# Performance work log

Measured on AMD Instinct MI355X. Metric: run time of the kernel, lower is better.

Reference implementation:

```python
import jax, jax.numpy as jnp
import numpy as np

B, R, N, M, K = 4, 4, 4096, 64, 3
F_NUM = 512
KN = K * N


def _block(x, Ws, bs):
    """SO-Net PointResNet: 1x1 convs + ReLU; last layer sees concat(input, hidden)."""
    h = x
    for W, b in zip(Ws[:-1], bs[:-1]):
        h = jax.nn.relu(jnp.einsum('oc,bcn->bon', W, h) + b[None, :, None])
    h = jnp.concatenate([x, h], axis=1)
    return jax.nn.relu(jnp.einsum('oc,bcn->bon', Ws[-1], h) + bs[-1][None, :, None])


def _forward(x, intensity, node, node_knn_I, fpW, fpB, gpW, gpB):
    # --- som.query_topk: k nearest SOM nodes per point ---
    xd = jax.lax.stop_gradient(x)
    dist = jnp.sum((xd[:, :, :, None] - node[:, :, None, :]) ** 2, axis=1)      # B,N,M
    _, topk = jax.lax.top_k(-dist, K)                                           # B,N,K
    min_idx = topk.transpose(0, 2, 1).reshape(B, KN)                            # B,KN (k copies stacked)
    mask = jax.nn.one_hot(min_idx, M, dtype=jnp.float32)                        # B,KN,M
    mask_row_max = jnp.max(mask, axis=1) > 0                                    # B,M  node has >=1 point
    mask_row_sum = jnp.sum(mask, axis=1)                                        # B,M  points per node

    x_stack = jnp.tile(x, (1, 1, K))                                            # B,2,KN
    cluster_mean = jnp.einsum('bcn,bnm->bcm', jax.lax.stop_gradient(x_stack), mask) \
                   / (mask_row_sum[:, None, :] + 1e-5)                          # B,2,M (detached)

    # --- rotation group (2x2 rotations at angles 2*pi*r/R) ---
    theta = 2.0 * jnp.pi * jnp.arange(R, dtype=jnp.float32) / R
    c, s = jnp.cos(theta), jnp.sin(theta)
    rot = jnp.stack([jnp.stack([c, -s], -1), jnp.stack([s, c], -1)], -2)        # R,2,2

    x_rot = jnp.einsum('rij,bjn->brin', rot, x_stack)                           # B,R,2,KN
    node_rot = jnp.einsum('rij,bjm->brim', rot, cluster_mean)                   # B,R,2,M
    centers = jnp.take_along_axis(node_rot, min_idx[:, None, None, :], axis=3)  # B,R,2,KN
    x_dec = jax.lax.stop_gradient(x_rot - centers).reshape(B * R, 2, KN)

    # --- first PointResNet over all B*R rotation copies ---
    feat = _block(x_dec, fpW, fpB)                                              # BR,128,KN

    # --- index_max scatter-max per SOM cluster (value of argmax == segment max) ---
    seg = jnp.tile(min_idx[:, None, :], (1, R, 1)).reshape(B * R, KN)
    segmax = jax.vmap(lambda f, sgi: jax.ops.segment_max(f.T, sgi, num_segments=M).T)(feat, seg)
    rowmax = jnp.tile(mask_row_max[:, None, :], (1, R, 1)).reshape(B * R, M)
    pooled = jnp.where(rowmax[:, None, :], segmax, feat[:, :, 0:1])             # BR,128,M (empty -> gather idx 0)

    # --- final PointResNet over SOM nodes, then max over nodes and rotations ---
    g_in = jnp.concatenate([node_rot.reshape(B * R, 2, M), pooled], axis=1)     # BR,130,M
    out = _block(g_in, gpW, gpB)                                                # BR,F,M
    return out.reshape(B, R, F_NUM, M).max(axis=3).max(axis=1)                  # B,F


def setup_inputs() -> dict:
    key = jax.random.key(0)
    ks = jax.random.split(key, 24)
    d = {}
    d['x'] = jax.random.normal(ks[0], (B, 2, N), jnp.float32)
    d['intensity'] = jax.random.uniform(ks[1], (B, 1, N), jnp.float32)
    d['node'] = jax.random.normal(ks[2], (B, 2, M), jnp.float32)
    d['node_knn_I'] = jax.random.randint(ks[3], (B, M, 1), 0, M)
    dims_fp = [(64, 2), (64, 64), (128, 64), (128, 130)]      # PointResNet(2,[64,64,128,128])
    dims_gp = [(256, 130), (256, 256), (512, 256), (F_NUM, 642)]  # PointResNet(130,[256,256,512,F])
    i = 4
    for name, dims in (('fp', dims_fp), ('gp', dims_gp)):
        for j, (o, ci) in enumerate(dims):
            d[f'{name}_W{j}'] = jax.random.normal(ks[i], (o, ci), jnp.float32) / np.sqrt(ci).astype(np.float32)
            d[f'{name}_b{j}'] = jnp.zeros((o,), jnp.float32)
            i += 1
    return d


def reference(x, intensity, node, node_knn_I,
              fp_W0, fp_b0, fp_W1, fp_b1, fp_W2, fp_b2, fp_W3, fp_b3,
              gp_W0, gp_b0, gp_W1, gp_b1, gp_W2, gp_b2, gp_W3, gp_b3):
    return _forward(x, intensity, node, node_knn_I,
                    [fp_W0, fp_W1, fp_W2, fp_W3], [fp_b0, fp_b1, fp_b2, fp_b3],
                    [gp_W0, gp_W1, gp_W2, gp_W3], [gp_b0, gp_b1, gp_b2, gp_b3])
```

## Files before the change

### kernel.cpp

```cpp
#include <hip/hip_runtime.h>
#include <stdint.h>

#define BB 4
#define RR 4
#define NN 4096
#define MM 64
#define KK 3
#define KNN 12288
#define BRR 16
#define FF 512

typedef short bf16x8 __attribute__((ext_vector_type(8)));
typedef float f32x4 __attribute__((ext_vector_type(4)));

__device__ __forceinline__ float bf2f(unsigned int u) {
  union { unsigned int i; float f; } v; v.i = u << 16; return v.f;
}
__device__ __forceinline__ unsigned short f2bf(float f) {
  union { float f; unsigned int i; } v; v.f = f;
  unsigned int x = v.i;
  return (unsigned short)((x + 0x7fffu + ((x >> 16) & 1u)) >> 16);
}
__device__ __forceinline__ float ldf(const void* p, long i, int isbf) {
  if (isbf) return bf2f(((const unsigned short*)p)[i]);
  return ((const float*)p)[i];
}

__global__ __launch_bounds__(256) void k_detect(
    const unsigned short* __restrict__ x, int* __restrict__ flag) {
  __shared__ int bad;
  if (threadIdx.x == 0) bad = 0;
  __syncthreads();
  int cnt = 0;
  for (int i = threadIdx.x; i < 1024; i += 256) {
    unsigned short u = x[i * 2];
    int e = (u >> 7) & 0xFF;
    if (e >= 0x90 || (e > 0 && e <= 0x50)) ++cnt;
  }
  atomicAdd(&bad, cnt);
  __syncthreads();
  if (threadIdx.x == 0) flag[0] = (bad < 100) ? 1 : 0;
}

struct WPtrs { const void* p[7]; };
__global__ __launch_bounds__(256) void k_cvt(
    WPtrs wp, const int* __restrict__ flag, unsigned short* __restrict__ Wb) {
  const int e0=4096, e1=12288, e2=28928, e3=62208, e4=127744, e5=258816, e6=587520;
  int t = blockIdx.x * 256 + threadIdx.x;
  if (t >= e6) return;
  int s, base;
  if      (t < e0) { s=0; base=0;  }
  else if (t < e1) { s=1; base=e0; }
  else if (t < e2) { s=2; base=e1; }
  else if (t < e3) { s=3; base=e2; }
  else if (t < e4) { s=4; base=e3; }
  else if (t < e5) { s=5; base=e4; }
  else             { s=6; base=e5; }
  int local = t - base;
  unsigned short u;
  if (flag[0]) u = ((const unsigned short*)wp.p[s])[local];
  else         u = f2bf(((const float*)wp.p[s])[local]);
  Wb[t] = u;
}

__global__ __launch_bounds__(256) void k_assign(
    const void* __restrict__ x, const void* __restrict__ node,
    const int* __restrict__ flag, int* __restrict__ idx, float* __restrict__ csum,
    int* __restrict__ blkcnt) {
  __shared__ float nd[2][64];
  __shared__ float cs[192];
  int isbf = flag[0];
  int tid = threadIdx.x;
  int b = blockIdx.x >> 4;
  int n = ((blockIdx.x & 15) << 8) + tid;
  if (tid < 128) nd[tid >> 6][tid & 63] = ldf(node, b * 128 + tid, isbf);
  if (tid < 192) cs[tid] = 0.f;
  __syncthreads();
  float x0 = ldf(x, b * 8192 + n, isbf);
  float x1 = ldf(x, b * 8192 + 4096 + n, isbf);
  float d0 = 1e30f, d1 = 1e30f, d2 = 1e30f;
  int m0 = 0, m1 = 0, m2 = 0;
#pragma unroll 8
  for (int m = 0; m < 64; ++m) {
    float dx = x0 - nd[0][m];
    float dy = x1 - nd[1][m];
    float d = __fmul_rn(dx, dx) + __fmul_rn(dy, dy);
    if (d < d0)      { d2=d1; m2=m1; d1=d0; m1=m0; d0=d; m0=m; }
    else if (d < d1) { d2=d1; m2=m1; d1=d;  m1=m; }
    else if (d < d2) { d2=d;  m2=m; }
  }
  long base = ((long)b * NN + n) * 3;
  idx[base] = m0; idx[base + 1] = m1; idx[base + 2] = m2;
  atomicAdd(&cs[m0*3+0], x0); atomicAdd(&cs[m0*3+1], x1); atomicAdd(&cs[m0*3+2], 1.f);
  atomicAdd(&cs[m1*3+0], x0); atomicAdd(&cs[m1*3+1], x1); atomicAdd(&cs[m1*3+2], 1.f);
  atomicAdd(&cs[m2*3+0], x0); atomicAdd(&cs[m2*3+1], x1); atomicAdd(&cs[m2*3+2], 1.f);
  __syncthreads();
  if (tid < 192) atomicAdd(&csum[b * 192 + tid], cs[tid]);
  if (tid < 64) blkcnt[blockIdx.x * 64 + tid] = (int)cs[tid*3 + 2];
}

__global__ __launch_bounds__(256) void k_means(
    const float* __restrict__ csum, const int* __restrict__ blkcnt,
    float* __restrict__ noderot, int* __restrict__ rowflag,
    int* __restrict__ off, int* __restrict__ blkoff) {
  int t = threadIdx.x;
  int b = t >> 6, m = t & 63;
  float s0 = csum[b*192 + m*3], s1 = csum[b*192 + m*3 + 1], c = csum[b*192 + m*3 + 2];
  float mx = s0 / (c + 1e-5f);
  float my = s1 / (c + 1e-5f);
  rowflag[b * 64 + m] = (c > 0.f) ? 1 : 0;
  for (int r = 0; r < 4; ++r) {
    float th = 1.5707964f * (float)r;
    float cr = cosf(th), sr = sinf(th);
    noderot[((b*4 + r)*2 + 0)*64 + m] = cr*mx - sr*my;
    noderot[((b*4 + r)*2 + 1)*64 + m] = sr*mx + cr*my;
  }
  if (m == 0) {
    int acc = 0;
    for (int mm = 0; mm < 64; ++mm) {
      off[b*64 + mm] = acc;
      acc += (int)csum[b*192 + mm*3 + 2];
    }
  }
  __syncthreads();
  int base = off[b*64 + m];
  for (int blk = 0; blk < 16; ++blk) {
    blkoff[(b*16 + blk)*64 + m] = base;
    base += blkcnt[(b*16 + blk)*64 + m];
  }
}

__global__ __launch_bounds__(256) void k_scatter(
    const int* __restrict__ idx, const int* __restrict__ blkoff,
    int* __restrict__ sorted) {
  __shared__ int lc[64];
  int tid = threadIdx.x;
  int blk = blockIdx.x;
  int b = blk >> 4;
  int n = ((blk & 15) << 8) + tid;
  if (tid < 64) lc[tid] = 0;
  __syncthreads();
#pragma unroll
  for (int kk = 0; kk < 3; ++kk) {
    int m = idx[((long)b * NN + n) * 3 + kk];
    int pos = atomicAdd(&lc[m], 1);
    sorted[b * KNN + blkoff[blk*64 + m] + pos] = (m << 12) | n;
  }
}

__global__ __launch_bounds__(256) void k_fused(
    const void* __restrict__ x, const int* __restrict__ sorted,
    const int* __restrict__ idx, const float* __restrict__ noderot,
    const int* __restrict__ flag,
    const void* __restrict__ fW0, const void* __restrict__ fb0,
    const unsigned short* __restrict__ Wb,
    const void* __restrict__ fb1, const void* __restrict__ fb2,
    const void* __restrict__ fb3,
    unsigned int* __restrict__ pooled, float* __restrict__ feat0) {
  __shared__ unsigned short Cs[64 * 136];
  __shared__ unsigned short Hs[64 * 72];
  __shared__ int mcol[64];
  const unsigned short* fW1 = Wb;
  const unsigned short* fW2 = Wb + 4096;
  const unsigned short* fW3 = Wb + 12288;
  int isbf = flag[0];
  int tid = threadIdx.x, lane = tid & 63, wv = tid >> 6;
  int quad = lane >> 4, lr = lane & 15;
  int br = blockIdx.y, b = br >> 2, r = br & 3;
  if (tid < 64) {
    int e = sorted[b * KNN + blockIdx.x * 64 + tid];
    int m = e >> 12, n = e & 4095;
    int isz = (n == 0 && m == idx[(long)b * NN * 3]) ? 256 : 0;
    mcol[tid] = m | isz;
    float x0 = ldf(x, b*8192 + n, isbf), x1 = ldf(x, b*8192 + 4096 + n, isbf);
    float th = 1.5707964f * (float)r;
    float cr = cosf(th), sr = sinf(th);
    float xd0 = (cr*x0 - sr*x1) - noderot[(br*2 + 0)*64 + m];
    float xd1 = (sr*x0 + cr*x1) - noderot[(br*2 + 1)*64 + m];
    *(unsigned int*)&Cs[tid * 136] = (unsigned int)f2bf(xd0) | ((unsigned int)f2bf(xd1) << 16);
  }
  __syncthreads();
  {
    int col = tid & 63, og = (tid >> 6) << 4;
    unsigned int xu = *(unsigned int*)&Cs[col * 136];
    float fx0 = bf2f(xu & 0xffff), fx1 = bf2f(xu >> 16);
    union { bf16x8 v; unsigned short s[8]; } o8[2];
#pragma unroll
    for (int j = 0; j < 16; ++j) {
      int o = og + j;
      float h = ldf(fb0, o, isbf) + ldf(fW0, o*2, isbf) * fx0 + ldf(fW0, o*2+1, isbf) * fx1;
      o8[j >> 3].s[j & 7] = f2bf(fmaxf(h, 0.f));
    }
    *(bf16x8*)&Hs[col*72 + og]     = o8[0].v;
    *(bf16x8*)&Hs[col*72 + og + 8] = o8[1].v;
  }
  __syncthreads();
  {
    int o0 = wv * 16;
    f32x4 acc[4];
    float bb4[4];
#pragma unroll
    for (int rr = 0; rr < 4; ++rr) bb4[rr] = ldf(fb1, o0 + quad*4 + rr, isbf);
#pragma unroll
    for (int nt = 0; nt < 4; ++nt) acc[nt] = (f32x4){bb4[0], bb4[1], bb4[2], bb4[3]};
#pragma unroll
    for (int ks = 0; ks < 64; ks += 32) {
      bf16x8 a = *(const bf16x8*)(fW1 + (o0 + lr)*64 + ks + quad*8);
#pragma unroll
      for (int nt = 0; nt < 4; ++nt) {
        bf16x8 bf = *(bf16x8*)&Hs[(nt*16 + lr)*72 + ks + quad*8];
        acc[nt] = __builtin_amdgcn_mfma_f32_16x16x32_bf16(a, bf, acc[nt], 0, 0, 0);
      }
    }
    __syncthreads();
#pragma unroll
    for (int nt = 0; nt < 4; ++nt) {
      int col = nt*16 + lr;
      union { unsigned long long u; unsigned short s[4]; } pk;
#pragma unroll
      for (int rr = 0; rr < 4; ++rr) pk.s[rr] = f2bf(fmaxf(acc[nt][rr], 0.f));
      *(unsigned long long*)&Hs[col*72 + o0 + quad*4] = pk.u;
    }
  }
  __syncthreads();
#pragma unroll
  for (int p2 = 0; p2 < 2; ++p2) {
    int o0 = p2*64 + wv*16;
    f32x4 acc[4];
    float bb4[4];
#pragma unroll
    for (int rr = 0; rr < 4; ++rr) bb4[rr] = ldf(fb2, o0 + quad*4 + rr, isbf);
#pragma unroll
    for (int nt = 0; nt < 4; ++nt) acc[nt] = (f32x4){bb4[0], bb4[1], bb4[2], bb4[3]};
#pragma unroll
    for (int ks = 0; ks < 64; ks += 32) {
      bf16x8 a = *(const bf16x8*)(fW2 + (o0 + lr)*64 + ks + quad*8);
#pragma unroll
      for (int nt = 0; nt < 4; ++nt) {
        bf16x8 bf = *(bf16x8*)&Hs[(nt*16 + lr)*72 + ks + quad*8];
        acc[nt] = __builtin_amdgcn_mfma_f32_16x16x32_bf16(a, bf, acc[nt], 0, 0, 0);
      }
    }
#pragma unroll
    for (int nt = 0; nt < 4; ++nt) {
      int col = nt*16 + lr;
      int o = o0 + quad*4;
      unsigned int w0 = (unsigned int)f2bf(fmaxf(acc[nt][0], 0.f)) |
                        ((unsigned int)f2bf(fmaxf(acc[nt][1], 0.f)) << 16);
      unsigned int w1 = (unsigned int)f2bf(fmaxf(acc[nt][2], 0.f)) |
                        ((unsigned int)f2bf(fmaxf(acc[nt][3], 0.f)) << 16);
      *(unsigned int*)&Cs[col*136 + 2 + o] = w0;
      *(unsigned int*)&Cs[col*136 + 4 + o] = w1;
    }
  }
  __syncthreads();
  f32x4 acc3[2][4];
#pragma unroll
  for (int p3 = 0; p3 < 2; ++p3) {
    int o0 = p3*64 + wv*16;
    float bb4[4];
#pragma unroll
    for (int rr = 0; rr < 4; ++rr) bb4[rr] = ldf(fb3, o0 + quad*4 + rr, isbf);
#pragma unroll
    for (int nt = 0; nt < 4; ++nt) acc3[p3][nt] = (f32x4){bb4[0], bb4[1], bb4[2], bb4[3]};
#pragma unroll
    for (int ks = 0; ks < 128; ks += 32) {
      union { bf16x8 v; unsigned int u[4]; } au;
      const unsigned int* ap = (const unsigned int*)(fW3 + (long)(o0 + lr)*130 + ks + quad*8);
      au.u[0] = ap[0]; au.u[1] = ap[1]; au.u[2] = ap[2]; au.u[3] = ap[3];
#pragma unroll
      for (int nt = 0; nt < 4; ++nt) {
        bf16x8 bf = *(bf16x8*)&Cs[(nt*16 + lr)*136 + ks + quad*8];
        acc3[p3][nt] = __builtin_amdgcn_mfma_f32_16x16x32_bf16(au.v, bf, acc3[p3][nt], 0, 0, 0);
      }
    }
#pragma unroll
    for (int rr = 0; rr < 4; ++rr) {
      int o = o0 + quad*4 + rr;
      unsigned int wu = *(const unsigned int*)(fW3 + (long)o*130 + 128);
      float w0 = bf2f(wu & 0xffff), w1 = bf2f(wu >> 16);
#pragma unroll
      for (int nt = 0; nt < 4; ++nt) {
        unsigned int bu = *(unsigned int*)&Cs[(nt*16 + lr)*136 + 128];
        acc3[p3][nt][rr] += w0 * bf2f(bu & 0xffff) + w1 * bf2f(bu >> 16);
      }
    }
  }
  __syncthreads();
#pragma unroll
  for (int p3 = 0; p3 < 2; ++p3) {
    int o0 = p3*64 + wv*16;
#pragma unroll
    for (int nt = 0; nt < 4; ++nt) {
      int col = nt*16 + lr;
      union { unsigned long long u; unsigned short s[4]; } pk;
#pragma unroll
      for (int rr = 0; rr < 4; ++rr) pk.s[rr] = f2bf(fmaxf(acc3[p3][nt][rr], 0.f));
      *(unsigned long long*)&Cs[col*136 + o0 + quad*4] = pk.u;
    }
  }
  __syncthreads();
  {
    int o = tid & 127, h = tid >> 7;
    int c0 = h * 32;
    int curm = mcol[c0] & 255;
    float v = 0.f;
    for (int c = c0; c < c0 + 32; ++c) {
      int mc = mcol[c];
      int mm = mc & 255;
      float f = bf2f(Cs[c*136 + o]);
      if (mm != curm) {
        atomicMax(&pooled[(((long)br*64 + curm) << 7) + o], __float_as_uint(v));
        curm = mm; v = 0.f;
      }
      v = fmaxf(v, f);
      if (mc & 256) feat0[br*128 + o] = f;
    }
    atomicMax(&pooled[(((long)br*64 + curm) << 7) + o], __float_as_uint(v));
  }
}

__global__ __launch_bounds__(256) void k_finalize(
    const unsigned int* __restrict__ pooled, const float* __restrict__ feat0,
    const int* __restrict__ rowflag, const float* __restrict__ noderot,
    unsigned short* __restrict__ AG) {
  int t = blockIdx.x * 256 + threadIdx.x;
  int col = t >> 7, o = t & 127;
  int br = col >> 6, m = col & 63, b = br >> 2;
  float v = __uint_as_float(pooled[((long)col << 7) + o]);
  if (!rowflag[b*64 + m]) v = feat0[br*128 + o];
  AG[(long)col*648 + 2 + o] = f2bf(v);
  if (o < 2) AG[(long)col*648 + o] = f2bf(noderot[(br*2 + o)*64 + m]);
}

template<int KW, int KMAIN, bool REM2, int BSTR, int OSTR, int OOFF, int EPI>
__global__ __launch_bounds__(256) void k_gemm(
    const unsigned short* __restrict__ W, const void* __restrict__ bias,
    const int* __restrict__ flag,
    const unsigned short* __restrict__ Bb, unsigned short* __restrict__ Out,
    unsigned int* __restrict__ outmax) {
  int isbf = flag[0];
  int lane = threadIdx.x & 63;
  int wv = threadIdx.x >> 6;
  int quad = lane >> 4, lr = lane & 15;
  int o0 = blockIdx.y * 64 + wv * 16;
  long p0 = (long)blockIdx.x * 64;
  float bia[4];
#pragma unroll
  for (int rr = 0; rr < 4; ++rr) bia[rr] = ldf(bias, o0 + quad*4 + rr, isbf);
  f32x4 acc[4];
#pragma unroll
  for (int nt = 0; nt < 4; ++nt) acc[nt] = (f32x4){bia[0], bia[1], bia[2], bia[3]};
  const unsigned short* arow = W + (long)(o0 + lr) * KW;
  for (int ks = 0; ks < KMAIN; ks += 32) {
    bf16x8 a;
    if constexpr ((KW % 8) == 0) {
      a = *(const bf16x8*)(arow + ks + quad*8);
    } else {
      union { bf16x8 v; unsigned int u[4]; } au;
      const unsigned int* ap = (const unsigned int*)(arow + ks + quad*8);
      au.u[0] = ap[0]; au.u[1] = ap[1]; au.u[2] = ap[2]; au.u[3] = ap[3];
      a = au.v;
    }
#pragma unroll
    for (int nt = 0; nt < 4; ++nt) {
      bf16x8 bf = *(const bf16x8*)(Bb + (p0 + nt*16 + lr) * BSTR + ks + quad*8);
      acc[nt] = __builtin_amdgcn_mfma_f32_16x16x32_bf16(a, bf, acc[nt], 0, 0, 0);
    }
  }
  if constexpr (REM2) {
#pragma unroll
    for (int rr = 0; rr < 4; ++rr) {
      int o = o0 + quad*4 + rr;
      unsigned int wu = *(const unsigned int*)(W + (long)o * KW + KMAIN);
      float w0 = bf2f(wu & 0xffff), w1 = bf2f(wu >> 16);
#pragma unroll
      for (int nt = 0; nt < 4; ++nt) {
        long p = p0 + nt*16 + lr;
        unsigned int bu = *(const unsigned int*)(Bb + p * BSTR + KMAIN);
        acc[nt][rr] += w0 * bf2f(bu & 0xffff) + w1 * bf2f(bu >> 16);
      }
    }
  }
  if constexpr (EPI == 0) {
#pragma unroll
    for (int nt = 0; nt < 4; ++nt) {
      long p = p0 + nt*16 + lr;
      unsigned short v0 = f2bf(fmaxf(acc[nt][0], 0.f));
      unsigned short v1 = f2bf(fmaxf(acc[nt][1], 0.f));
      unsigned short v2 = f2bf(fmaxf(acc[nt][2], 0.f));
      unsigned short v3 = f2bf(fmaxf(acc[nt][3], 0.f));
      unsigned short* op = Out + p * OSTR + OOFF + o0 + quad*4;
      if constexpr (((OOFF * 2) % 8) == 0) {
        union { unsigned long long u; unsigned short s[4]; } pk;
        pk.s[0] = v0; pk.s[1] = v1; pk.s[2] = v2; pk.s[3] = v3;
        *(unsigned long long*)op = pk.u;
      } else {
        *(unsigned int*)op       = (unsigned int)v0 | ((unsigned int)v1 << 16);
        *(unsigned int*)(op + 2) = (unsigned int)v2 | ((unsigned int)v3 << 16);
      }
    }
  } else {
#pragma unroll
    for (int rr = 0; rr < 4; ++rr) {
      float v = fmaxf(fmaxf(acc[0][rr], acc[1][rr]), fmaxf(acc[2][rr], acc[3][rr]));
      v = fmaxf(v, 0.f);
      v = fmaxf(v, __shfl_xor(v, 1, 64));
      v = fmaxf(v, __shfl_xor(v, 2, 64));
      v = fmaxf(v, __shfl_xor(v, 4, 64));
      v = fmaxf(v, __shfl_xor(v, 8, 64));
      if (lr == 0) {
        int bb2 = (int)(blockIdx.x >> 2);
        atomicMax(&outmax[bb2 * FF + o0 + quad*4 + rr], __float_as_uint(v));
      }
    }
  }
}

__global__ __launch_bounds__(256) void k_out(
    const unsigned int* __restrict__ outmax, const int* __restrict__ flag,
    void* __restrict__ out) {
  int t = blockIdx.x * 256 + threadIdx.x;
  float v = __uint_as_float(outmax[t]);
  if (flag[0]) ((unsigned short*)out)[t] = f2bf(v);
  else         ((float*)out)[t] = v;
}

extern "C" void kernel_launch(void* const* d_in, const int* in_sizes, int n_in,
                              void* d_out, int out_size, void* d_ws, size_t ws_size,
                              hipStream_t stream) {
  const void* x    = d_in[0];
  const void* node = d_in[2];
  const void* fpW0 = d_in[4];  const void* fpb0 = d_in[5];
  const void* fpW1 = d_in[6];  const void* fpb1 = d_in[7];
  const void* fpW2 = d_in[8];  const void* fpb2 = d_in[9];
  const void* fpW3 = d_in[10]; const void* fpb3 = d_in[11];
  const void* gpW0 = d_in[12]; const void* gpb0 = d_in[13];
  const void* gpW1 = d_in[14]; const void* gpb1 = d_in[15];
  const void* gpW2 = d_in[16]; const void* gpb2 = d_in[17];
  const void* gpW3 = d_in[18]; const void* gpb3 = d_in[19];

  char* ws = (char*)d_ws;
  int*            flag    = (int*)(ws + 0);
  float*          csum    = (float*)(ws + 256);
  unsigned int*   outmax  = (unsigned int*)(ws + 3328);
  unsigned int*   pooled  = (unsigned int*)(ws + 11520);
  int*            idx     = (int*)(ws + 535808);
  int*            blkcnt  = (int*)(ws + 732416);
  int*            blkoff  = (int*)(ws + 748800);
  int*            off     = (int*)(ws + 765184);
  float*          noderot = (float*)(ws + 766208);
  int*            rowflag = (int*)(ws + 774400);
  int*            sorted  = (int*)(ws + 775424);
  float*          feat0   = (float*)(ws + 972032);
  unsigned short* AG      = (unsigned short*)(ws + 980224);
  unsigned short* Hg1     = (unsigned short*)(ws + 2307328);
  unsigned short* Hg2     = (unsigned short*)(ws + 2831616);
  unsigned short* Wb      = (unsigned short*)(ws + 3355904);

  hipMemsetAsync(ws, 0, 535808, stream);

  k_detect<<<1, 256, 0, stream>>>((const unsigned short*)x, flag);
  WPtrs wp; wp.p[0]=fpW1; wp.p[1]=fpW2; wp.p[2]=fpW3; wp.p[3]=gpW0;
  wp.p[4]=gpW1; wp.p[5]=gpW2; wp.p[6]=gpW3;
  k_cvt<<<2295, 256, 0, stream>>>(wp, flag, Wb);

  k_assign<<<64, 256, 0, stream>>>(x, node, flag, idx, csum, blkcnt);
  k_means<<<1, 256, 0, stream>>>(csum, blkcnt, noderot, rowflag, off, blkoff);
  k_scatter<<<64, 256, 0, stream>>>(idx, blkoff, sorted);
  k_fused<<<dim3(192, 16), 256, 0, stream>>>(x, sorted, idx, noderot, flag,
                                             fpW0, fpb0, Wb, fpb1, fpb2, fpb3,
                                             pooled, feat0);
  k_finalize<<<512, 256, 0, stream>>>(pooled, feat0, rowflag, noderot, AG);

  const unsigned short* gW0 = Wb + 28928;
  const unsigned short* gW1 = Wb + 62208;
  const unsigned short* gW2 = Wb + 127744;
  const unsigned short* gW3 = Wb + 258816;
  k_gemm<130, 128, true, 648, 256, 0, 0><<<dim3(16, 4), 256, 0, stream>>>(gW0, gpb0, flag, AG, Hg1, nullptr);
  k_gemm<256, 256, false, 256, 256, 0, 0><<<dim3(16, 4), 256, 0, stream>>>(gW1, gpb1, flag, Hg1, Hg2, nullptr);
  k_gemm<256, 256, false, 256, 648, 130, 0><<<dim3(16, 8), 256, 0, stream>>>(gW2, gpb2, flag, Hg2, AG, nullptr);
  k_gemm<642, 640, true, 648, 0, 0, 2><<<dim3(16, 8), 256, 0, stream>>>(gW3, gpb3, flag, AG, nullptr, outmax);

  k_out<<<8, 256, 0, stream>>>(outmax, flag, d_out);
}
```

Measured before the change: 201.0 us.

## Fuse launch pipeline into four kernels with a single-block-tile global-pool MLP

```diff
diff --git a/kernel.cpp b/kernel.cpp
--- a/kernel.cpp
+++ b/kernel.cpp
@@ -10,6 +10,24 @@
 #define BRR 16
 #define FF 512
 
+#define W_FPW1 0
+#define W_FPW2 4096
+#define W_FPW3 12288
+#define W_GPW0 28928
+#define W_GPW1 62208
+#define W_GPW2 127744
+#define W_GPW3 258816
+#define W_FPB1 587520
+#define W_FPB2 587584
+#define W_FPB3 587712
+#define W_GPB0 587840
+#define W_GPB1 588096
+#define W_GPB2 588352
+#define W_GPB3 588864
+#define W_FPB0 589376
+#define W_FPW0 589440
+#define W_TOT  589568
+
 typedef short bf16x8 __attribute__((ext_vector_type(8)));
 typedef float f32x4 __attribute__((ext_vector_type(4)));
 
@@ -21,56 +39,68 @@
   unsigned int x = v.i;
   return (unsigned short)((x + 0x7fffu + ((x >> 16) & 1u)) >> 16);
 }
+__device__ __forceinline__ unsigned int f2bf2(float a, float b) {
+#if __has_builtin(__builtin_amdgcn_cvt_pk_bf16_f32)
+  typedef __bf16 bf2_t __attribute__((ext_vector_type(2)));
+  union { bf2_t v; unsigned int u; } c;
+  c.v = __builtin_amdgcn_cvt_pk_bf16_f32(a, b);
+  return c.u;
+#else
+  return (unsigned int)f2bf(a) | ((unsigned int)f2bf(b) << 16);
+#endif
+}
 __device__ __forceinline__ float ldf(const void* p, long i, int isbf) {
   if (isbf) return bf2f(((const unsigned short*)p)[i]);
   return ((const float*)p)[i];
 }
-
-__global__ __launch_bounds__(256) void k_detect(
-    const unsigned short* __restrict__ x, int* __restrict__ flag) {
-  __shared__ int bad;
-  if (threadIdx.x == 0) bad = 0;
-  __syncthreads();
-  int cnt = 0;
-  for (int i = threadIdx.x; i < 1024; i += 256) {
-    unsigned short u = x[i * 2];
-    int e = (u >> 7) & 0xFF;
-    if (e >= 0x90 || (e > 0 && e <= 0x50)) ++cnt;
-  }
-  atomicAdd(&bad, cnt);
-  __syncthreads();
-  if (threadIdx.x == 0) flag[0] = (bad < 100) ? 1 : 0;
-}
-
-struct WPtrs { const void* p[7]; };
-__global__ __launch_bounds__(256) void k_cvt(
-    WPtrs wp, const int* __restrict__ flag, unsigned short* __restrict__ Wb) {
-  const int e0=4096, e1=12288, e2=28928, e3=62208, e4=127744, e5=258816, e6=587520;
-  int t = blockIdx.x * 256 + threadIdx.x;
-  if (t >= e6) return;
-  int s, base;
-  if      (t < e0) { s=0; base=0;  }
-  else if (t < e1) { s=1; base=e0; }
-  else if (t < e2) { s=2; base=e1; }
-  else if (t < e3) { s=3; base=e2; }
-  else if (t < e4) { s=4; base=e3; }
-  else if (t < e5) { s=5; base=e4; }
-  else             { s=6; base=e5; }
-  int local = t - base;
-  unsigned short u;
-  if (flag[0]) u = ((const unsigned short*)wp.p[s])[local];
-  else         u = f2bf(((const float*)wp.p[s])[local]);
-  Wb[t] = u;
-}
-
-__global__ __launch_bounds__(256) void k_assign(
-    const void* __restrict__ x, const void* __restrict__ node,
-    const int* __restrict__ flag, int* __restrict__ idx, float* __restrict__ csum,
-    int* __restrict__ blkcnt) {
+__device__ __forceinline__ int detect_bf(const unsigned short* xs) {
+  int lane = threadIdx.x & 63;
+  unsigned short u = xs[lane * 2];
+  int e = (u >> 7) & 0xFF;
+  int bad = (e >= 0x90 || (e > 0 && e <= 0x50)) ? 1 : 0;
+  unsigned long long m = __ballot(bad);
+  return __popcll(m) < 16;
+}
+
+struct SrcPtrs { const void* p[16]; };
+__global__ __launch_bounds__(256) void k_pre(
+    SrcPtrs sp, const void* __restrict__ x, const void* __restrict__ node,
+    int* __restrict__ idx, float* __restrict__ csum, int* __restrict__ blkcnt,
+    unsigned short* __restrict__ Wb) {
+  int isbf = detect_bf((const unsigned short*)x);
+  int tid = threadIdx.x;
+  if (blockIdx.x >= 64) {
+    int t = (blockIdx.x - 64) * 256 + tid;
+    if (t >= W_TOT) return;
+    int s, base;
+    if (t < 28928) {
+      if (t < 4096)        { s=0;  base=0; }
+      else if (t < 12288)  { s=1;  base=4096; }
+      else                 { s=2;  base=12288; }
+    } else if (t < 587520) {
+      if (t < 62208)       { s=3;  base=28928; }
+      else if (t < 127744) { s=4;  base=62208; }
+      else if (t < 258816) { s=5;  base=127744; }
+      else                 { s=6;  base=258816; }
+    } else if (t < 588864) {
+      if (t < 587584)      { s=7;  base=587520; }
+      else if (t < 587712) { s=8;  base=587584; }
+      else if (t < 587840) { s=9;  base=587712; }
+      else if (t < 588096) { s=10; base=587840; }
+      else if (t < 588352) { s=11; base=588096; }
+      else                 { s=12; base=588352; }
+    } else {
+      if (t < 589376)      { s=13; base=588864; }
+      else if (t < 589440) { s=14; base=589376; }
+      else                 { s=15; base=589440; }
+    }
+    int local = t - base;
+    Wb[t] = isbf ? ((const unsigned short*)sp.p[s])[local]
+                 : f2bf(((const float*)sp.p[s])[local]);
+    return;
+  }
   __shared__ float nd[2][64];
   __shared__ float cs[192];
-  int isbf = flag[0];
-  int tid = threadIdx.x;
   int b = blockIdx.x >> 4;
   int n = ((blockIdx.x & 15) << 8) + tid;
   if (tid < 128) nd[tid >> 6][tid & 63] = ldf(node, b * 128 + tid, isbf);
@@ -99,71 +129,70 @@
   if (tid < 64) blkcnt[blockIdx.x * 64 + tid] = (int)cs[tid*3 + 2];
 }
 
-__global__ __launch_bounds__(256) void k_means(
+__global__ __launch_bounds__(256) void k_mid(
     const float* __restrict__ csum, const int* __restrict__ blkcnt,
+    const int* __restrict__ idx,
     float* __restrict__ noderot, int* __restrict__ rowflag,
-    int* __restrict__ off, int* __restrict__ blkoff) {
-  int t = threadIdx.x;
-  int b = t >> 6, m = t & 63;
-  float s0 = csum[b*192 + m*3], s1 = csum[b*192 + m*3 + 1], c = csum[b*192 + m*3 + 2];
-  float mx = s0 / (c + 1e-5f);
-  float my = s1 / (c + 1e-5f);
-  rowflag[b * 64 + m] = (c > 0.f) ? 1 : 0;
-  for (int r = 0; r < 4; ++r) {
-    float th = 1.5707964f * (float)r;
-    float cr = cosf(th), sr = sinf(th);
-    noderot[((b*4 + r)*2 + 0)*64 + m] = cr*mx - sr*my;
-    noderot[((b*4 + r)*2 + 1)*64 + m] = sr*mx + cr*my;
-  }
-  if (m == 0) {
-    int acc = 0;
-    for (int mm = 0; mm < 64; ++mm) {
-      off[b*64 + mm] = acc;
-      acc += (int)csum[b*192 + mm*3 + 2];
-    }
-  }
-  __syncthreads();
-  int base = off[b*64 + m];
-  for (int blk = 0; blk < 16; ++blk) {
-    blkoff[(b*16 + blk)*64 + m] = base;
-    base += blkcnt[(b*16 + blk)*64 + m];
-  }
-}
-
-__global__ __launch_bounds__(256) void k_scatter(
-    const int* __restrict__ idx, const int* __restrict__ blkoff,
     int* __restrict__ sorted) {
+  __shared__ float cls[192];
+  __shared__ int offs[64];
+  __shared__ int lbase[64];
   __shared__ int lc[64];
   int tid = threadIdx.x;
   int blk = blockIdx.x;
-  int b = blk >> 4;
-  int n = ((blk & 15) << 8) + tid;
-  if (tid < 64) lc[tid] = 0;
-  __syncthreads();
+  int b = blk >> 4, chunk = blk & 15;
+  if (tid < 192) cls[tid] = csum[b * 192 + tid];
+  __syncthreads();
+  if (tid < 64) {
+    int m = tid;
+    float s0 = cls[m*3], s1 = cls[m*3+1], c = cls[m*3+2];
+    float mx = s0 / (c + 1e-5f), my = s1 / (c + 1e-5f);
+    rowflag[b*64 + m] = (c > 0.f) ? 1 : 0;
+    for (int r = 0; r < 4; ++r) {
+      float th = 1.5707964f * (float)r;
+      float cr = cosf(th), sr = sinf(th);
+      noderot[((b*4+r)*2+0)*64 + m] = cr*mx - sr*my;
+      noderot[((b*4+r)*2+1)*64 + m] = sr*mx + cr*my;
+    }
+    lc[m] = 0;
+  }
+  if (tid == 0) {
+    int acc = 0;
+    for (int mm = 0; mm < 64; ++mm) { offs[mm] = acc; acc += (int)cls[mm*3+2]; }
+  }
+  __syncthreads();
+  if (tid < 64) {
+    int base = offs[tid];
+    for (int c2 = 0; c2 < chunk; ++c2) base += blkcnt[(b*16 + c2)*64 + tid];
+    lbase[tid] = base;
+  }
+  __syncthreads();
+  int n = (chunk << 8) + tid;
 #pragma unroll
   for (int kk = 0; kk < 3; ++kk) {
-    int m = idx[((long)b * NN + n) * 3 + kk];
+    int m = idx[((long)b*NN + n)*3 + kk];
     int pos = atomicAdd(&lc[m], 1);
-    sorted[b * KNN + blkoff[blk*64 + m] + pos] = (m << 12) | n;
+    sorted[b*KNN + lbase[m] + pos] = (m << 12) | n;
   }
 }
 
 __global__ __launch_bounds__(256) void k_fused(
     const void* __restrict__ x, const int* __restrict__ sorted,
     const int* __restrict__ idx, const float* __restrict__ noderot,
-    const int* __restrict__ flag,
-    const void* __restrict__ fW0, const void* __restrict__ fb0,
     const unsigned short* __restrict__ Wb,
-    const void* __restrict__ fb1, const void* __restrict__ fb2,
-    const void* __restrict__ fb3,
     unsigned int* __restrict__ pooled, float* __restrict__ feat0) {
   __shared__ unsigned short Cs[64 * 136];
   __shared__ unsigned short Hs[64 * 72];
   __shared__ int mcol[64];
-  const unsigned short* fW1 = Wb;
-  const unsigned short* fW2 = Wb + 4096;
-  const unsigned short* fW3 = Wb + 12288;
-  int isbf = flag[0];
+  const unsigned short* fW1 = Wb + W_FPW1;
+  const unsigned short* fW2 = Wb + W_FPW2;
+  const unsigned short* fW3 = Wb + W_FPW3;
+  const unsigned short* fb1 = Wb + W_FPB1;
+  const unsigned short* fb2 = Wb + W_FPB2;
+  const unsigned short* fb3 = Wb + W_FPB3;
+  const unsigned short* fb0 = Wb + W_FPB0;
+  const unsigned short* fW0 = Wb + W_FPW0;
+  int isbf = detect_bf((const unsigned short*)x);
   int tid = threadIdx.x, lane = tid & 63, wv = tid >> 6;
   int quad = lane >> 4, lr = lane & 15;
   int br = blockIdx.y, b = br >> 2, r = br & 3;
@@ -177,22 +206,25 @@
     float cr = cosf(th), sr = sinf(th);
     float xd0 = (cr*x0 - sr*x1) - noderot[(br*2 + 0)*64 + m];
     float xd1 = (sr*x0 + cr*x1) - noderot[(br*2 + 1)*64 + m];
-    *(unsigned int*)&Cs[tid * 136] = (unsigned int)f2bf(xd0) | ((unsigned int)f2bf(xd1) << 16);
+    *(unsigned int*)&Cs[tid * 136] = f2bf2(xd0, xd1);
   }
   __syncthreads();
   {
     int col = tid & 63, og = (tid >> 6) << 4;
     unsigned int xu = *(unsigned int*)&Cs[col * 136];
     float fx0 = bf2f(xu & 0xffff), fx1 = bf2f(xu >> 16);
-    union { bf16x8 v; unsigned short s[8]; } o8[2];
-#pragma unroll
-    for (int j = 0; j < 16; ++j) {
+    union { unsigned int u[8]; bf16x8 v[2]; } o8;
+#pragma unroll
+    for (int j = 0; j < 16; j += 2) {
       int o = og + j;
-      float h = ldf(fb0, o, isbf) + ldf(fW0, o*2, isbf) * fx0 + ldf(fW0, o*2+1, isbf) * fx1;
-      o8[j >> 3].s[j & 7] = f2bf(fmaxf(h, 0.f));
-    }
-    *(bf16x8*)&Hs[col*72 + og]     = o8[0].v;
-    *(bf16x8*)&Hs[col*72 + og + 8] = o8[1].v;
+      unsigned int wu0 = *(const unsigned int*)&fW0[o*2];
+      unsigned int wu1 = *(const unsigned int*)&fW0[o*2 + 2];
+      float h0 = bf2f(fb0[o])   + bf2f(wu0 & 0xffff)*fx0 + bf2f(wu0 >> 16)*fx1;
+      float h1 = bf2f(fb0[o+1]) + bf2f(wu1 & 0xffff)*fx0 + bf2f(wu1 >> 16)*fx1;
+      o8.u[j >> 1] = f2bf2(fmaxf(h0, 0.f), fmaxf(h1, 0.f));
+    }
+    *(bf16x8*)&Hs[col*72 + og]     = o8.v[0];
+    *(bf16x8*)&Hs[col*72 + og + 8] = o8.v[1];
   }
   __syncthreads();
   {
@@ -200,7 +232,7 @@
     f32x4 acc[4];
     float bb4[4];
 #pragma unroll
-    for (int rr = 0; rr < 4; ++rr) bb4[rr] = ldf(fb1, o0 + quad*4 + rr, isbf);
+    for (int rr = 0; rr < 4; ++rr) bb4[rr] = bf2f(fb1[o0 + quad*4 + rr]);
 #pragma unroll
     for (int nt = 0; nt < 4; ++nt) acc[nt] = (f32x4){bb4[0], bb4[1], bb4[2], bb4[3]};
 #pragma unroll
@@ -216,10 +248,10 @@
 #pragma unroll
     for (int nt = 0; nt < 4; ++nt) {
       int col = nt*16 + lr;
-      union { unsigned long long u; unsigned short s[4]; } pk;
-#pragma unroll
-      for (int rr = 0; rr < 4; ++rr) pk.s[rr] = f2bf(fmaxf(acc[nt][rr], 0.f));
-      *(unsigned long long*)&Hs[col*72 + o0 + quad*4] = pk.u;
+      unsigned long long pk =
+        (unsigned long long)f2bf2(fmaxf(acc[nt][0],0.f), fmaxf(acc[nt][1],0.f)) |
+        ((unsigned long long)f2bf2(fmaxf(acc[nt][2],0.f), fmaxf(acc[nt][3],0.f)) << 32);
+      *(unsigned long long*)&Hs[col*72 + o0 + quad*4] = pk;
     }
   }
   __syncthreads();
@@ -229,7 +261,7 @@
     f32x4 acc[4];
     float bb4[4];
 #pragma unroll
-    for (int rr = 0; rr < 4; ++rr) bb4[rr] = ldf(fb2, o0 + quad*4 + rr, isbf);
+    for (int rr = 0; rr < 4; ++rr) bb4[rr] = bf2f(fb2[o0 + quad*4 + rr]);
 #pragma unroll
     for (int nt = 0; nt < 4; ++nt) acc[nt] = (f32x4){bb4[0], bb4[1], bb4[2], bb4[3]};
 #pragma unroll
@@ -245,12 +277,8 @@
     for (int nt = 0; nt < 4; ++nt) {
       int col = nt*16 + lr;
       int o = o0 + quad*4;
-      unsigned int w0 = (unsigned int)f2bf(fmaxf(acc[nt][0], 0.f)) |
-                        ((unsigned int)f2bf(fmaxf(acc[nt][1], 0.f)) << 16);
-      unsigned int w1 = (unsigned int)f2bf(fmaxf(acc[nt][2], 0.f)) |
-                        ((unsigned int)f2bf(fmaxf(acc[nt][3], 0.f)) << 16);
-      *(unsigned int*)&Cs[col*136 + 2 + o] = w0;
-      *(unsigned int*)&Cs[col*136 + 4 + o] = w1;
+      *(unsigned int*)&Cs[col*136 + 2 + o] = f2bf2(fmaxf(acc[nt][0],0.f), fmaxf(acc[nt][1],0.f));
+      *(unsigned int*)&Cs[col*136 + 4 + o] = f2bf2(fmaxf(acc[nt][2],0.f), fmaxf(acc[nt][3],0.f));
     }
   }
   __syncthreads();
@@ -260,7 +288,7 @@
     int o0 = p3*64 + wv*16;
     float bb4[4];
 #pragma unroll
-    for (int rr = 0; rr < 4; ++rr) bb4[rr] = ldf(fb3, o0 + quad*4 + rr, isbf);
+    for (int rr = 0; rr < 4; ++rr) bb4[rr] = bf2f(fb3[o0 + quad*4 + rr]);
 #pragma unroll
     for (int nt = 0; nt < 4; ++nt) acc3[p3][nt] = (f32x4){bb4[0], bb4[1], bb4[2], bb4[3]};
 #pragma unroll
@@ -293,10 +321,10 @@
 #pragma unroll
     for (int nt = 0; nt < 4; ++nt) {
       int col = nt*16 + lr;
-      union { unsigned long long u; unsigned short s[4]; } pk;
-#pragma unroll
-      for (int rr = 0; rr < 4; ++rr) pk.s[rr] = f2bf(fmaxf(acc3[p3][nt][rr], 0.f));
-      *(unsigned long long*)&Cs[col*136 + o0 + quad*4] = pk.u;
+      unsigned long long pk =
+        (unsigned long long)f2bf2(fmaxf(acc3[p3][nt][0],0.f), fmaxf(acc3[p3][nt][1],0.f)) |
+        ((unsigned long long)f2bf2(fmaxf(acc3[p3][nt][2],0.f), fmaxf(acc3[p3][nt][3],0.f)) << 32);
+      *(unsigned long long*)&Cs[col*136 + o0 + quad*4] = pk;
     }
   }
   __syncthreads();
@@ -320,110 +348,179 @@
   }
 }
 
-__global__ __launch_bounds__(256) void k_finalize(
+__global__ __launch_bounds__(256) void k_gp(
+    const void* __restrict__ x,
     const unsigned int* __restrict__ pooled, const float* __restrict__ feat0,
     const int* __restrict__ rowflag, const float* __restrict__ noderot,
-    unsigned short* __restrict__ AG) {
-  int t = blockIdx.x * 256 + threadIdx.x;
-  int col = t >> 7, o = t & 127;
-  int br = col >> 6, m = col & 63, b = br >> 2;
-  float v = __uint_as_float(pooled[((long)col << 7) + o]);
-  if (!rowflag[b*64 + m]) v = feat0[br*128 + o];
-  AG[(long)col*648 + 2 + o] = f2bf(v);
-  if (o < 2) AG[(long)col*648 + o] = f2bf(noderot[(br*2 + o)*64 + m]);
-}
-
-template<int KW, int KMAIN, bool REM2, int BSTR, int OSTR, int OOFF, int EPI>
-__global__ __launch_bounds__(256) void k_gemm(
-    const unsigned short* __restrict__ W, const void* __restrict__ bias,
-    const int* __restrict__ flag,
-    const unsigned short* __restrict__ Bb, unsigned short* __restrict__ Out,
-    unsigned int* __restrict__ outmax) {
-  int isbf = flag[0];
-  int lane = threadIdx.x & 63;
-  int wv = threadIdx.x >> 6;
+    const unsigned short* __restrict__ Wb,
+    unsigned int* __restrict__ outmax, unsigned int* __restrict__ counter,
+    void* __restrict__ out) {
+  __shared__ unsigned short AGs[16 * 648];
+  __shared__ unsigned short H1s[16 * 264];
+  __shared__ unsigned short H2s[16 * 264];
+  __shared__ int done_s;
+  int isbf = detect_bf((const unsigned short*)x);
+  int tid = threadIdx.x, lane = tid & 63, wv = tid >> 6;
   int quad = lane >> 4, lr = lane & 15;
-  int o0 = blockIdx.y * 64 + wv * 16;
-  long p0 = (long)blockIdx.x * 64;
-  float bia[4];
-#pragma unroll
-  for (int rr = 0; rr < 4; ++rr) bia[rr] = ldf(bias, o0 + quad*4 + rr, isbf);
-  f32x4 acc[4];
-#pragma unroll
-  for (int nt = 0; nt < 4; ++nt) acc[nt] = (f32x4){bia[0], bia[1], bia[2], bia[3]};
-  const unsigned short* arow = W + (long)(o0 + lr) * KW;
-  for (int ks = 0; ks < KMAIN; ks += 32) {
-    bf16x8 a;
-    if constexpr ((KW % 8) == 0) {
-      a = *(const bf16x8*)(arow + ks + quad*8);
-    } else {
-      union { bf16x8 v; unsigned int u[4]; } au;
-      const unsigned int* ap = (const unsigned int*)(arow + ks + quad*8);
-      au.u[0] = ap[0]; au.u[1] = ap[1]; au.u[2] = ap[2]; au.u[3] = ap[3];
-      a = au.v;
-    }
-#pragma unroll
-    for (int nt = 0; nt < 4; ++nt) {
-      bf16x8 bf = *(const bf16x8*)(Bb + (p0 + nt*16 + lr) * BSTR + ks + quad*8);
-      acc[nt] = __builtin_amdgcn_mfma_f32_16x16x32_bf16(a, bf, acc[nt], 0, 0, 0);
-    }
-  }
-  if constexpr (REM2) {
-#pragma unroll
-    for (int rr = 0; rr < 4; ++rr) {
-      int o = o0 + quad*4 + rr;
-      unsigned int wu = *(const unsigned int*)(W + (long)o * KW + KMAIN);
-      float w0 = bf2f(wu & 0xffff), w1 = bf2f(wu >> 16);
-#pragma unroll
-      for (int nt = 0; nt < 4; ++nt) {
-        long p = p0 + nt*16 + lr;
-        unsigned int bu = *(const unsigned int*)(Bb + p * BSTR + KMAIN);
-        acc[nt][rr] += w0 * bf2f(bu & 0xffff) + w1 * bf2f(bu >> 16);
-      }
-    }
-  }
-  if constexpr (EPI == 0) {
-#pragma unroll
-    for (int nt = 0; nt < 4; ++nt) {
-      long p = p0 + nt*16 + lr;
-      unsigned short v0 = f2bf(fmaxf(acc[nt][0], 0.f));
-      unsigned short v1 = f2bf(fmaxf(acc[nt][1], 0.f));
-      unsigned short v2 = f2bf(fmaxf(acc[nt][2], 0.f));
-      unsigned short v3 = f2bf(fmaxf(acc[nt][3], 0.f));
-      unsigned short* op = Out + p * OSTR + OOFF + o0 + quad*4;
-      if constexpr (((OOFF * 2) % 8) == 0) {
-        union { unsigned long long u; unsigned short s[4]; } pk;
-        pk.s[0] = v0; pk.s[1] = v1; pk.s[2] = v2; pk.s[3] = v3;
-        *(unsigned long long*)op = pk.u;
-      } else {
-        *(unsigned int*)op       = (unsigned int)v0 | ((unsigned int)v1 << 16);
-        *(unsigned int*)(op + 2) = (unsigned int)v2 | ((unsigned int)v3 << 16);
-      }
-    }
-  } else {
-#pragma unroll
-    for (int rr = 0; rr < 4; ++rr) {
-      float v = fmaxf(fmaxf(acc[0][rr], acc[1][rr]), fmaxf(acc[2][rr], acc[3][rr]));
-      v = fmaxf(v, 0.f);
-      v = fmaxf(v, __shfl_xor(v, 1, 64));
-      v = fmaxf(v, __shfl_xor(v, 2, 64));
-      v = fmaxf(v, __shfl_xor(v, 4, 64));
-      v = fmaxf(v, __shfl_xor(v, 8, 64));
-      if (lr == 0) {
-        int bb2 = (int)(blockIdx.x >> 2);
-        atomicMax(&outmax[bb2 * FF + o0 + quad*4 + rr], __float_as_uint(v));
-      }
-    }
-  }
-}
-
-__global__ __launch_bounds__(256) void k_out(
-    const unsigned int* __restrict__ outmax, const int* __restrict__ flag,
-    void* __restrict__ out) {
-  int t = blockIdx.x * 256 + threadIdx.x;
-  float v = __uint_as_float(outmax[t]);
-  if (flag[0]) ((unsigned short*)out)[t] = f2bf(v);
-  else         ((float*)out)[t] = v;
+  int col0 = blockIdx.x * 16;
+  int br = col0 >> 6, b = br >> 2;
+  for (int i = tid; i < 2048; i += 256) {
+    int c = i >> 7, o = i & 127;
+    int gc = col0 + c, m = gc & 63;
+    float v = __uint_as_float(pooled[((long)gc << 7) + o]);
+    if (!rowflag[b * 64 + m]) v = feat0[br * 128 + o];
+    AGs[c * 648 + 2 + o] = f2bf(v);
+  }
+  if (tid < 32) {
+    int c = tid >> 1, j = tid & 1;
+    int m = (col0 + c) & 63;
+    AGs[c * 648 + j] = f2bf(noderot[(br * 2 + j) * 64 + m]);
+  }
+  __syncthreads();
+  {
+    const unsigned short* W = Wb + W_GPW0;
+    const unsigned short* Bi = Wb + W_GPB0;
+    f32x4 acc[4];
+#pragma unroll
+    for (int rt = 0; rt < 4; ++rt) {
+      int o0 = wv*64 + rt*16 + quad*4;
+      acc[rt] = (f32x4){bf2f(Bi[o0]), bf2f(Bi[o0+1]), bf2f(Bi[o0+2]), bf2f(Bi[o0+3])};
+    }
+#pragma unroll
+    for (int ks = 0; ks < 128; ks += 32) {
+      bf16x8 bfr = *(bf16x8*)&AGs[lr * 648 + ks + quad * 8];
+#pragma unroll
+      for (int rt = 0; rt < 4; ++rt) {
+        int o0 = wv*64 + rt*16;
+        union { bf16x8 v; unsigned int u[4]; } au;
+        const unsigned int* ap = (const unsigned int*)(W + (o0 + lr)*130 + ks + quad*8);
+        au.u[0]=ap[0]; au.u[1]=ap[1]; au.u[2]=ap[2]; au.u[3]=ap[3];
+        acc[rt] = __builtin_amdgcn_mfma_f32_16x16x32_bf16(au.v, bfr, acc[rt], 0,0,0);
+      }
+    }
+    unsigned int bu = *(unsigned int*)&AGs[lr * 648 + 128];
+    float b0v = bf2f(bu & 0xffff), b1v = bf2f(bu >> 16);
+#pragma unroll
+    for (int rt = 0; rt < 4; ++rt) {
+#pragma unroll
+      for (int rr = 0; rr < 4; ++rr) {
+        int o = wv*64 + rt*16 + quad*4 + rr;
+        unsigned int wu = *(const unsigned int*)(W + o*130 + 128);
+        acc[rt][rr] += bf2f(wu & 0xffff)*b0v + bf2f(wu >> 16)*b1v;
+      }
+      int o0 = wv*64 + rt*16;
+      unsigned long long pk =
+        (unsigned long long)f2bf2(fmaxf(acc[rt][0],0.f), fmaxf(acc[rt][1],0.f)) |
+        ((unsigned long long)f2bf2(fmaxf(acc[rt][2],0.f), fmaxf(acc[rt][3],0.f)) << 32);
+      *(unsigned long long*)&H1s[lr*264 + o0 + quad*4] = pk;
+    }
+  }
+  __syncthreads();
+  {
+    const unsigned short* W = Wb + W_GPW1;
+    const unsigned short* Bi = Wb + W_GPB1;
+    f32x4 acc[4];
+#pragma unroll
+    for (int rt = 0; rt < 4; ++rt) {
+      int o0 = wv*64 + rt*16 + quad*4;
+      acc[rt] = (f32x4){bf2f(Bi[o0]), bf2f(Bi[o0+1]), bf2f(Bi[o0+2]), bf2f(Bi[o0+3])};
+    }
+    for (int ks = 0; ks < 256; ks += 32) {
+      bf16x8 bfr = *(bf16x8*)&H1s[lr * 264 + ks + quad * 8];
+#pragma unroll
+      for (int rt = 0; rt < 4; ++rt) {
+        int o0 = wv*64 + rt*16;
+        bf16x8 a = *(const bf16x8*)(W + (o0 + lr)*256 + ks + quad*8);
+        acc[rt] = __builtin_amdgcn_mfma_f32_16x16x32_bf16(a, bfr, acc[rt], 0,0,0);
+      }
+    }
+#pragma unroll
+    for (int rt = 0; rt < 4; ++rt) {
+      int o0 = wv*64 + rt*16;
+      unsigned long long pk =
+        (unsigned long long)f2bf2(fmaxf(acc[rt][0],0.f), fmaxf(acc[rt][1],0.f)) |
+        ((unsigned long long)f2bf2(fmaxf(acc[rt][2],0.f), fmaxf(acc[rt][3],0.f)) << 32);
+      *(unsigned long long*)&H2s[lr*264 + o0 + quad*4] = pk;
+    }
+  }
+  __syncthreads();
+  {
+    const unsigned short* W = Wb + W_GPW2;
+    const unsigned short* Bi = Wb + W_GPB2;
+    f32x4 acc[8];
+#pragma unroll
+    for (int rt = 0; rt < 8; ++rt) {
+      int o0 = wv*128 + rt*16 + quad*4;
+      acc[rt] = (f32x4){bf2f(Bi[o0]), bf2f(Bi[o0+1]), bf2f(Bi[o0+2]), bf2f(Bi[o0+3])};
+    }
+    for (int ks = 0; ks < 256; ks += 32) {
+      bf16x8 bfr = *(bf16x8*)&H2s[lr * 264 + ks + quad * 8];
+#pragma unroll
+      for (int rt = 0; rt < 8; ++rt) {
+        int o0 = wv*128 + rt*16;
+        bf16x8 a = *(const bf16x8*)(W + (o0 + lr)*256 + ks + quad*8);
+        acc[rt] = __builtin_amdgcn_mfma_f32_16x16x32_bf16(a, bfr, acc[rt], 0,0,0);
+      }
+    }
+#pragma unroll
+    for (int rt = 0; rt < 8; ++rt) {
+      int o0 = wv*128 + rt*16;
+      *(unsigned int*)&AGs[lr*648 + 130 + o0 + quad*4] =
+          f2bf2(fmaxf(acc[rt][0],0.f), fmaxf(acc[rt][1],0.f));
+      *(unsigned int*)&AGs[lr*648 + 132 + o0 + quad*4] =
+          f2bf2(fmaxf(acc[rt][2],0.f), fmaxf(acc[rt][3],0.f));
+    }
+  }
+  __syncthreads();
+  {
+    const unsigned short* W = Wb + W_GPW3;
+    const unsigned short* Bi = Wb + W_GPB3;
+    f32x4 acc[8];
+#pragma unroll
+    for (int rt = 0; rt < 8; ++rt) {
+      int o0 = wv*128 + rt*16 + quad*4;
+      acc[rt] = (f32x4){bf2f(Bi[o0]), bf2f(Bi[o0+1]), bf2f(Bi[o0+2]), bf2f(Bi[o0+3])};
+    }
+    for (int ks = 0; ks < 640; ks += 32) {
+      bf16x8 bfr = *(bf16x8*)&AGs[lr * 648 + ks + quad * 8];
+#pragma unroll
+      for (int rt = 0; rt < 8; ++rt) {
+        int o0 = wv*128 + rt*16;
+        union { bf16x8 v; unsigned int u[4]; } au;
+        const unsigned int* ap = (const unsigned int*)(W + (long)(o0 + lr)*642 + ks + quad*8);
+        au.u[0]=ap[0]; au.u[1]=ap[1]; au.u[2]=ap[2]; au.u[3]=ap[3];
+        acc[rt] = __builtin_amdgcn_mfma_f32_16x16x32_bf16(au.v, bfr, acc[rt], 0,0,0);
+      }
+    }
+    unsigned int bu = *(unsigned int*)&AGs[lr * 648 + 640];
+    float b0v = bf2f(bu & 0xffff), b1v = bf2f(bu >> 16);
+#pragma unroll
+    for (int rt = 0; rt < 8; ++rt) {
+#pragma unroll
+      for (int rr = 0; rr < 4; ++rr) {
+        int o = wv*128 + rt*16 + quad*4 + rr;
+        unsigned int wu = *(const unsigned int*)(W + (long)o*642 + 640);
+        float v = acc[rt][rr] + bf2f(wu & 0xffff)*b0v + bf2f(wu >> 16)*b1v;
+        v = fmaxf(v, 0.f);
+        v = fmaxf(v, __shfl_xor(v, 1, 64));
+        v = fmaxf(v, __shfl_xor(v, 2, 64));
+        v = fmaxf(v, __shfl_xor(v, 4, 64));
+        v = fmaxf(v, __shfl_xor(v, 8, 64));
+        if (lr == 0) atomicMax(&outmax[b * FF + o], __float_as_uint(v));
+      }
+    }
+  }
+  __threadfence();
+  __syncthreads();
+  if (tid == 0) done_s = (int)atomicAdd(counter, 1u);
+  __syncthreads();
+  if (done_s == 63) {
+    for (int t = tid; t < 2048; t += 256) {
+      float v = __uint_as_float(atomicMax(&outmax[t], 0u));
+      if (isbf) ((unsigned short*)out)[t] = f2bf(v);
+      else      ((float*)out)[t] = v;
+    }
+  }
 }
 
 extern "C" void kernel_launch(void* const* d_in, const int* in_sizes, int n_in,
@@ -431,56 +528,43 @@
                               hipStream_t stream) {
   const void* x    = d_in[0];
   const void* node = d_in[2];
-  const void* fpW0 = d_in[4];  const void* fpb0 = d_in[5];
-  const void* fpW1 = d_in[6];  const void* fpb1 = d_in[7];
-  const void* fpW2 = d_in[8];  const void* fpb2 = d_in[9];
-  const void* fpW3 = d_in[10]; const void* fpb3 = d_in[11];
-  const void* gpW0 = d_in[12]; const void* gpb0 = d_in[13];
-  const void* gpW1 = d_in[14]; const void* gpb1 = d_in[15];
-  const void* gpW2 = d_in[16]; const void* gpb2 = d_in[17];
-  const void* gpW3 = d_in[18]; const void* gpb3 = d_in[19];
 
   char* ws = (char*)d_ws;
-  int*            flag    = (int*)(ws + 0);
-  float*          csum    = (float*)(ws + 256);
-  unsigned int*   outmax  = (unsigned int*)(ws + 3328);
+  float*          csum    = (float*)(ws + 0);
+  unsigned int*   outmax  = (unsigned int*)(ws + 3072);
+  unsigned int*   counter = (unsigned int*)(ws + 11264);
   unsigned int*   pooled  = (unsigned int*)(ws + 11520);
   int*            idx     = (int*)(ws + 535808);
   int*            blkcnt  = (int*)(ws + 732416);
-  int*            blkoff  = (int*)(ws + 748800);
-  int*            off     = (int*)(ws + 765184);
-  float*          noderot = (float*)(ws + 766208);
-  int*            rowflag = (int*)(ws + 774400);
-  int*            sorted  = (int*)(ws + 775424);
-  float*          feat0   = (float*)(ws + 972032);
-  unsigned short* AG      = (unsigned short*)(ws + 980224);
-  unsigned short* Hg1     = (unsigned short*)(ws + 2307328);
-  unsigned short* Hg2     = (unsigned short*)(ws + 2831616);
-  unsigned short* Wb      = (unsigned short*)(ws + 3355904);
+  float*          noderot = (float*)(ws + 748800);
+  int*            rowflag = (int*)(ws + 756992);
+  int*            sorted  = (int*)(ws + 758016);
+  float*          feat0   = (float*)(ws + 954624);
+  unsigned short* Wb      = (unsigned short*)(ws + 962816);
 
   hipMemsetAsync(ws, 0, 535808, stream);
 
-  k_detect<<<1, 256, 0, stream>>>((const unsigned short*)x, flag);
-  WPtrs wp; wp.p[0]=fpW1; wp.p[1]=fpW2; wp.p[2]=fpW3; wp.p[3]=gpW0;
-  wp.p[4]=gpW1; wp.p[5]=gpW2; wp.p[6]=gpW3;
-  k_cvt<<<2295, 256, 0, stream>>>(wp, flag, Wb);
-
-  k_assign<<<64, 256, 0, stream>>>(x, node, flag, idx, csum, blkcnt);
-  k_means<<<1, 256, 0, stream>>>(csum, blkcnt, noderot, rowflag, off, blkoff);
-  k_scatter<<<64, 256, 0, stream>>>(idx, blkoff, sorted);
-  k_fused<<<dim3(192, 16), 256, 0, stream>>>(x, sorted, idx, noderot, flag,
-                                             fpW0, fpb0, Wb, fpb1, fpb2, fpb3,
-                                             pooled, feat0);
-  k_finalize<<<512, 256, 0, stream>>>(pooled, feat0, rowflag, noderot, AG);
-
-  const unsigned short* gW0 = Wb + 28928;
-  const unsigned short* gW1 = Wb + 62208;
-  const unsigned short* gW2 = Wb + 127744;
-  const unsigned short* gW3 = Wb + 258816;
-  k_gemm<130, 128, true, 648, 256, 0, 0><<<dim3(16, 4), 256, 0, stream>>>(gW0, gpb0, flag, AG, Hg1, nullptr);
-  k_gemm<256, 256, false, 256, 256, 0, 0><<<dim3(16, 4), 256, 0, stream>>>(gW1, gpb1, flag, Hg1, Hg2, nullptr);
-  k_gemm<256, 256, false, 256, 648, 130, 0><<<dim3(16, 8), 256, 0, stream>>>(gW2, gpb2, flag, Hg2, AG, nullptr);
-  k_gemm<642, 640, true, 648, 0, 0, 2><<<dim3(16, 8), 256, 0, stream>>>(gW3, gpb3, flag, AG, nullptr, outmax);
-
-  k_out<<<8, 256, 0, stream>>>(outmax, flag, d_out);
-}
+  SrcPtrs sp;
+  sp.p[0]  = d_in[6];
+  sp.p[1]  = d_in[8];
+  sp.p[2]  = d_in[10];
+  sp.p[3]  = d_in[12];
+  sp.p[4]  = d_in[14];
+  sp.p[5]  = d_in[16];
+  sp.p[6]  = d_in[18];
+  sp.p[7]  = d_in[7];
+  sp.p[8]  = d_in[9];
+  sp.p[9]  = d_in[11];
+  sp.p[10] = d_in[13];
+  sp.p[11] = d_in[15];
+  sp.p[12] = d_in[17];
+  sp.p[13] = d_in[19];
+  sp.p[14] = d_in[5];
+  sp.p[15] = d_in[4];
+
+  k_pre<<<64 + (W_TOT + 255) / 256, 256, 0, stream>>>(sp, x, node, idx, csum, blkcnt, Wb);
+  k_mid<<<64, 256, 0, stream>>>(csum, blkcnt, idx, noderot, rowflag, sorted);
+  k_fused<<<dim3(192, 16), 256, 0, stream>>>(x, sorted, idx, noderot, Wb, pooled, feat0);
+  k_gp<<<64, 256, 0, stream>>>(x, pooled, feat0, rowflag, noderot, Wb,
+                               outmax, counter, d_out);
+}
```

Result: slower. 245.2 us (+22.0%).
